# Optimization experiments

Hardware: AMD Instinct MI355X
Metric: run time of the kernel (lower is better)

## Reference

```python
import jax, jax.numpy as jnp
import numpy as np

N_NODES = 100000
N_EDGES = 1250000
D_IN = 64
D_HID = 64
N_CLS = 40


def setup_inputs() -> dict:
    key = jax.random.key(0)
    ks = jax.random.split(key, 8)
    x = jax.random.normal(ks[0], (N_NODES, D_IN), dtype=jnp.float32)
    edge_index = jax.random.randint(ks[1], (2, N_EDGES), 0, N_NODES, dtype=jnp.int64)
    s = 1.0 / np.sqrt(D_IN)
    W1_l = jax.random.normal(ks[2], (D_IN, D_HID), dtype=jnp.float32) * s
    W1_r = jax.random.normal(ks[3], (D_IN, D_HID), dtype=jnp.float32) * s
    b1 = jnp.zeros((D_HID,), dtype=jnp.float32)
    s2 = 1.0 / np.sqrt(D_HID)
    W2_l = jax.random.normal(ks[4], (D_HID, N_CLS), dtype=jnp.float32) * s2
    W2_r = jax.random.normal(ks[5], (D_HID, N_CLS), dtype=jnp.float32) * s2
    b2 = jnp.zeros((N_CLS,), dtype=jnp.float32)
    return {"x": x, "edge_index": edge_index, "W1_l": W1_l, "b1": b1,
            "W1_r": W1_r, "W2_l": W2_l, "b2": b2, "W2_r": W2_r}


def _sage_conv(h, src, dst, n_nodes, W_l, b, W_r):
    # mean-aggregate neighbor features: out[i] = mean_{(j->i)} h[j]
    msg = h[src]                                             # [E, d] gather
    agg = jax.ops.segment_sum(msg, dst, num_segments=n_nodes)  # [N, d] scatter-add
    deg = jax.ops.segment_sum(jnp.ones_like(dst, dtype=h.dtype), dst,
                              num_segments=n_nodes)
    agg = agg / jnp.maximum(deg, 1.0)[:, None]
    # lin_l(aggregated, bias) + lin_r(root, no bias)
    return agg @ W_l + b + h @ W_r


def reference(x, edge_index, W1_l, b1, W1_r, W2_l, b2, W2_r):
    n = x.shape[0]
    src, dst = edge_index[0], edge_index[1]
    h = jax.nn.relu(_sage_conv(x, src, dst, n, W1_l, b1, W1_r))
    # dropout is identity in eval mode (training=False)
    h = _sage_conv(h, src, dst, n, W2_l, b2, W2_r)
    return jax.nn.log_softmax(h, axis=1)
```

## Files before the change

kernel.cpp:

```cpp
#include <hip/hip_runtime.h>
#include <hip/hip_bf16.h>
#include <math.h>

#define N_NODES 100000
#define N_EDGES 1250000
#define D_IN    64
#define D_HID   64
#define N_CLS   40

#define NBUCK      500
#define BUCK_NODES 200
#define BUCK_CAP   2944
#define NBLK_STAGE 512
#define NBLK_GEMM1 1024
#define ELL_W      44

typedef unsigned int uint;
typedef __attribute__((ext_vector_type(8))) short bf16x8;
typedef __attribute__((ext_vector_type(4))) float f32x4;

static __device__ __forceinline__ uint pack_bf16x2(float a, float b) {
    unsigned short ua = __builtin_bit_cast(unsigned short, __float2bfloat16(a));
    unsigned short ub = __builtin_bit_cast(unsigned short, __float2bfloat16(b));
    return (uint)ua | ((uint)ub << 16);
}
static __device__ __forceinline__ short f2bf(float f) {
    return (short)__builtin_bit_cast(unsigned short, __float2bfloat16(f));
}

__global__ __launch_bounds__(256, 3) void stage_and_gemm1(
    const int* __restrict__ src, const int* __restrict__ dst,
    int* __restrict__ bucketCnt, uint* __restrict__ staged,
    const float* __restrict__ x,
    const float* __restrict__ W_l, const float* __restrict__ W_r,
    const float* __restrict__ b,
    __hip_bfloat16* __restrict__ y1, __hip_bfloat16* __restrict__ r1,
    int ntiles)
{
    __shared__ int cntB[NBUCK], offB[NBUCK], gbase[NBUCK];

    if (blockIdx.x < NBLK_STAGE) {
        const int per = (N_EDGES + NBLK_STAGE - 1) / NBLK_STAGE;
        const int e0 = blockIdx.x * per;
        const int e1 = (e0 + per < N_EDGES) ? e0 + per : N_EDGES;
        for (int i = threadIdx.x; i < NBUCK; i += 256) { cntB[i] = 0; offB[i] = 0; }
        __syncthreads();
        for (int e = e0 + threadIdx.x; e < e1; e += 256)
            atomicAdd(&cntB[dst[e] / BUCK_NODES], 1);
        __syncthreads();
        for (int i = threadIdx.x; i < NBUCK; i += 256) {
            int c = cntB[i];
            gbase[i] = c ? atomicAdd(&bucketCnt[i], c) : 0;
        }
        __syncthreads();
        for (int e = e0 + threadIdx.x; e < e1; e += 256) {
            int d = dst[e];
            int s = src[e];
            int bk = d / BUCK_NODES;
            int pos = gbase[bk] + atomicAdd(&offB[bk], 1);
            if (pos < BUCK_CAP)
                staged[(size_t)bk * BUCK_CAP + pos] =
                    (uint)s | ((uint)(d - bk * BUCK_NODES) << 17);
        }
        return;
    }

    const int gbid = blockIdx.x - NBLK_STAGE;
    if (gbid == 0 && threadIdx.x < 64)
        y1[(size_t)N_NODES * 64 + threadIdx.x] = __float2bfloat16(0.0f);

    const int lane = threadIdx.x & 63;
    const int m = lane & 15;
    const int q = lane >> 4;

    bf16x8 bfrag[8][2];
    float  biasv[4];
    #pragma unroll
    for (int t = 0; t < 8; ++t) {
        const float* Wsrc = (t < 4) ? W_l : W_r;
        const int c = t * 16 + m - ((t < 4) ? 0 : 64);
        #pragma unroll
        for (int ks = 0; ks < 2; ++ks) {
            bf16x8 f;
            #pragma unroll
            for (int j = 0; j < 8; ++j)
                f[j] = f2bf(Wsrc[(ks * 32 + q * 8 + j) * 64 + c]);
            bfrag[t][ks] = f;
        }
    }
    #pragma unroll
    for (int t = 0; t < 4; ++t) biasv[t] = b[t * 16 + m];

    int wid = gbid * 4 + (threadIdx.x >> 6);
    const int nw = NBLK_GEMM1 * 4;
    for (int tile = wid; tile < ntiles; tile += nw) {
        const int node0 = tile * 16;
        const float* xrow = x + (size_t)(node0 + m) * 64 + q * 8;
        bf16x8 afrag[2];
        #pragma unroll
        for (int ks = 0; ks < 2; ++ks) {
            float4 f0 = *(const float4*)(xrow + ks * 32);
            float4 f1 = *(const float4*)(xrow + ks * 32 + 4);
            bf16x8 a;
            a[0] = f2bf(f0.x); a[1] = f2bf(f0.y); a[2] = f2bf(f0.z); a[3] = f2bf(f0.w);
            a[4] = f2bf(f1.x); a[5] = f2bf(f1.y); a[6] = f2bf(f1.z); a[7] = f2bf(f1.w);
            afrag[ks] = a;
        }
        f32x4 acc[8];
        #pragma unroll
        for (int t = 0; t < 8; ++t) acc[t] = (f32x4){0.f, 0.f, 0.f, 0.f};
        #pragma unroll
        for (int ks = 0; ks < 2; ++ks) {
            #pragma unroll
            for (int t = 0; t < 8; ++t)
                acc[t] = __builtin_amdgcn_mfma_f32_16x16x32_bf16(
                    afrag[ks], bfrag[t][ks], acc[t], 0, 0, 0);
        }
        #pragma unroll
        for (int t = 0; t < 8; ++t) {
            #pragma unroll
            for (int r = 0; r < 4; ++r) {
                const size_t row = (size_t)(node0 + q * 4 + r);
                if (t < 4)
                    y1[row * 64 + t * 16 + m] = __float2bfloat16(acc[t][r]);
                else
                    r1[row * 64 + (t - 4) * 16 + m] =
                        __float2bfloat16(acc[t][r] + biasv[t - 4]);
            }
        }
    }
}

__global__ __launch_bounds__(256) void ell_fill(
    const uint* __restrict__ staged, const int* __restrict__ bucketCnt,
    int* __restrict__ cnt, int* __restrict__ slots)
{
    __shared__ int lcnt[BUCK_NODES];
    const int b = blockIdx.x;
    const int node0 = b * BUCK_NODES;
    for (int i = threadIdx.x; i < BUCK_NODES; i += 256) lcnt[i] = 0;
    __syncthreads();
    int total = bucketCnt[b];
    if (total > BUCK_CAP) total = BUCK_CAP;
    const uint* sp = staged + (size_t)b * BUCK_CAP;
    for (int i = threadIdx.x; i < total; i += 256) {
        uint v = sp[i];
        int off = (int)(v >> 17);
        int pos = atomicAdd(&lcnt[off], 1);
        if (pos < ELL_W)
            slots[(size_t)(node0 + off) * ELL_W + pos] = (int)(v & 0x1FFFFu);
    }
    __syncthreads();
    for (int i = threadIdx.x; i < BUCK_NODES; i += 256) {
        int node = node0 + i;
        if (node < N_NODES) cnt[node] = lcnt[i];
    }
}

__global__ __launch_bounds__(256, 3) void gemm2_mfma(
    const __hip_bfloat16* __restrict__ h,
    const float* __restrict__ W_l, const float* __restrict__ W_r,
    const float* __restrict__ b,
    __hip_bfloat16* __restrict__ y2, __hip_bfloat16* __restrict__ r2,
    int ntiles)
{
    if (blockIdx.x == 0 && threadIdx.x < N_CLS)
        y2[(size_t)N_NODES * N_CLS + threadIdx.x] = __float2bfloat16(0.0f);

    const int lane = threadIdx.x & 63;
    const int m = lane & 15;
    const int q = lane >> 4;

    bf16x8 bfrag[5][2];
    float  biasv[5];
    #pragma unroll
    for (int t = 0; t < 5; ++t) {
        const int g = t * 16 + m;
        const float* Wsrc = (g < N_CLS) ? W_l : W_r;
        const int c = (g < N_CLS) ? g : g - N_CLS;
        #pragma unroll
        for (int ks = 0; ks < 2; ++ks) {
            bf16x8 f;
            #pragma unroll
            for (int j = 0; j < 8; ++j)
                f[j] = f2bf(Wsrc[(ks * 32 + q * 8 + j) * N_CLS + c]);
            bfrag[t][ks] = f;
        }
        biasv[t] = (g >= N_CLS) ? b[g - N_CLS] : 0.0f;
    }

    int wid = blockIdx.x * 4 + (threadIdx.x >> 6);
    const int nw = gridDim.x * 4;
    for (int tile = wid; tile < ntiles; tile += nw) {
        const int node0 = tile * 16;
        const __hip_bfloat16* hrow = h + (size_t)(node0 + m) * 64 + q * 8;
        bf16x8 afrag[2];
        afrag[0] = *(const bf16x8*)(hrow);
        afrag[1] = *(const bf16x8*)(hrow + 32);
        f32x4 acc[5];
        #pragma unroll
        for (int t = 0; t < 5; ++t) acc[t] = (f32x4){0.f, 0.f, 0.f, 0.f};
        #pragma unroll
        for (int ks = 0; ks < 2; ++ks) {
            #pragma unroll
            for (int t = 0; t < 5; ++t)
                acc[t] = __builtin_amdgcn_mfma_f32_16x16x32_bf16(
                    afrag[ks], bfrag[t][ks], acc[t], 0, 0, 0);
        }
        #pragma unroll
        for (int t = 0; t < 5; ++t) {
            const int g = t * 16 + m;
            #pragma unroll
            for (int r = 0; r < 4; ++r) {
                const size_t row = (size_t)(node0 + q * 4 + r);
                float v = acc[t][r] + biasv[t];
                if (g < N_CLS) y2[row * N_CLS + g] = __float2bfloat16(v);
                else           r2[row * N_CLS + (g - N_CLS)] = __float2bfloat16(v);
            }
        }
    }
}

__global__ __launch_bounds__(256, 8) void gather1(
    const __hip_bfloat16* __restrict__ y1,
    const int* __restrict__ cnt, const int* __restrict__ slots,
    __hip_bfloat16* __restrict__ h,
    int n_nodes)
{
    const int lane = threadIdx.x & 63;
    const int q4  = (lane >> 4) * 4;
    const int pre = (lane & 15) * 8;
    const char* y1c = (const char*)y1;

    const int wave = blockIdx.x * 4 + (threadIdx.x >> 6);
    const int nw   = gridDim.x * 4;

    int node = wave;
    if (node >= n_nodes) return;
    int degr = cnt[node];
    int idxv = slots[node * ELL_W + lane];

    for (;;) {
        const int nnode = node + nw;
        int ndeg = 0, nidx = 0;
        if (nnode < n_nodes) {
            ndeg = cnt[nnode];
            nidx = slots[nnode * ELL_W + lane];
        }

        const int degc = degr < ELL_W ? degr : ELL_W;
        int idx = (lane >= degc) ? n_nodes : idxv;
        float a0 = 0.f, a1 = 0.f, a2 = 0.f, a3 = 0.f;
        const int groups = (degc + 15) & ~15;
        for (int e = 0; e < groups; e += 16) {
            int sel0 = __builtin_amdgcn_ds_bpermute(e * 4      + q4, idx);
            int sel1 = __builtin_amdgcn_ds_bpermute(e * 4 + 16 + q4, idx);
            int sel2 = __builtin_amdgcn_ds_bpermute(e * 4 + 32 + q4, idx);
            int sel3 = __builtin_amdgcn_ds_bpermute(e * 4 + 48 + q4, idx);
            uint2 d0 = *(const uint2*)(y1c + ((size_t)(uint)sel0 * 128u + (uint)pre));
            uint2 d1 = *(const uint2*)(y1c + ((size_t)(uint)sel1 * 128u + (uint)pre));
            uint2 d2 = *(const uint2*)(y1c + ((size_t)(uint)sel2 * 128u + (uint)pre));
            uint2 d3 = *(const uint2*)(y1c + ((size_t)(uint)sel3 * 128u + (uint)pre));
            a0 += __uint_as_float(d0.x << 16) + __uint_as_float(d1.x << 16)
                + __uint_as_float(d2.x << 16) + __uint_as_float(d3.x << 16);
            a1 += __uint_as_float(d0.x & 0xffff0000u) + __uint_as_float(d1.x & 0xffff0000u)
                + __uint_as_float(d2.x & 0xffff0000u) + __uint_as_float(d3.x & 0xffff0000u);
            a2 += __uint_as_float(d0.y << 16) + __uint_as_float(d1.y << 16)
                + __uint_as_float(d2.y << 16) + __uint_as_float(d3.y << 16);
            a3 += __uint_as_float(d0.y & 0xffff0000u) + __uint_as_float(d1.y & 0xffff0000u)
                + __uint_as_float(d2.y & 0xffff0000u) + __uint_as_float(d3.y & 0xffff0000u);
        }
        a0 += __shfl_xor(a0, 16); a0 += __shfl_xor(a0, 32);
        a1 += __shfl_xor(a1, 16); a1 += __shfl_xor(a1, 32);
        a2 += __shfl_xor(a2, 16); a2 += __shfl_xor(a2, 32);
        a3 += __shfl_xor(a3, 16); a3 += __shfl_xor(a3, 32);

        uint2 rr = *(const uint2*)((const char*)h + ((size_t)node * 128u + (uint)pre));
        float r0  = __uint_as_float(rr.x << 16);
        float r1v = __uint_as_float(rr.x & 0xffff0000u);
        float r2v = __uint_as_float(rr.y << 16);
        float r3  = __uint_as_float(rr.y & 0xffff0000u);

        float inv = 1.0f / (float)(degr > 1 ? degr : 1);
        float v0 = a0 * inv + r0;  v0 = v0 > 0.f ? v0 : 0.f;
        float v1 = a1 * inv + r1v; v1 = v1 > 0.f ? v1 : 0.f;
        float v2 = a2 * inv + r2v; v2 = v2 > 0.f ? v2 : 0.f;
        float v3 = a3 * inv + r3;  v3 = v3 > 0.f ? v3 : 0.f;

        if (lane < 16) {
            uint2 o;
            o.x = pack_bf16x2(v0, v1);
            o.y = pack_bf16x2(v2, v3);
            *(uint2*)((char*)h + ((size_t)node * 128u + (uint)pre)) = o;
        }

        if (nnode >= n_nodes) break;
        node = nnode; degr = ndeg; idxv = nidx;
    }
}

__global__ __launch_bounds__(256, 8) void gather2(
    const __hip_bfloat16* __restrict__ y2,
    const __hip_bfloat16* __restrict__ r2,
    const int* __restrict__ cnt, const int* __restrict__ slots,
    float* __restrict__ out, int n_nodes)
{
    const int lane  = threadIdx.x & 63;
    const int lpair = lane & 31;
    const int p2    = (lane >> 5) * 4;
    const int pre2  = (lpair < 20 ? lpair : 19) * 4;
    const char* y2c = (const char*)y2;

    const int wave = blockIdx.x * 4 + (threadIdx.x >> 6);
    const int nw   = gridDim.x * 4;

    int node = wave;
    if (node >= n_nodes) return;
    int degr = cnt[node];
    int idxv = slots[node * ELL_W + lane];

    for (;;) {
        const int nnode = node + nw;
        int ndeg = 0, nidx = 0;
        if (nnode < n_nodes) {
            ndeg = cnt[nnode];
            nidx = slots[nnode * ELL_W + lane];
        }

        const int degc = degr < ELL_W ? degr : ELL_W;
        int idx = (lane >= degc) ? n_nodes : idxv;
        float a0 = 0.f, a1 = 0.f;
        const int groups = (degc + 7) & ~7;
        for (int e = 0; e < groups; e += 8) {
            int sel0 = __builtin_amdgcn_ds_bpermute(e * 4      + p2, idx);
            int sel1 = __builtin_amdgcn_ds_bpermute(e * 4 +  8 + p2, idx);
            int sel2 = __builtin_amdgcn_ds_bpermute(e * 4 + 16 + p2, idx);
            int sel3 = __builtin_amdgcn_ds_bpermute(e * 4 + 24 + p2, idx);
            uint d0 = *(const uint*)(y2c + ((size_t)(uint)sel0 * 80u + (uint)pre2));
            uint d1 = *(const uint*)(y2c + ((size_t)(uint)sel1 * 80u + (uint)pre2));
            uint d2 = *(const uint*)(y2c + ((size_t)(uint)sel2 * 80u + (uint)pre2));
            uint d3 = *(const uint*)(y2c + ((size_t)(uint)sel3 * 80u + (uint)pre2));
            a0 += __uint_as_float(d0 << 16) + __uint_as_float(d1 << 16)
                + __uint_as_float(d2 << 16) + __uint_as_float(d3 << 16);
            a1 += __uint_as_float(d0 & 0xffff0000u) + __uint_as_float(d1 & 0xffff0000u)
                + __uint_as_float(d2 & 0xffff0000u) + __uint_as_float(d3 & 0xffff0000u);
        }
        a0 += __shfl_xor(a0, 32);
        a1 += __shfl_xor(a1, 32);

        uint rr = *(const uint*)((const char*)r2 + ((size_t)node * 80u + (uint)pre2));
        float r0 = __uint_as_float(rr << 16);
        float r1 = __uint_as_float(rr & 0xffff0000u);

        float inv = 1.0f / (float)(degr > 1 ? degr : 1);
        float l0 = a0 * inv + r0;
        float l1 = a1 * inv + r1;
        if (lpair >= 20) { l0 = -INFINITY; l1 = -INFINITY; }

        float m = fmaxf(l0, l1);
        #pragma unroll
        for (int off = 16; off > 0; off >>= 1)
            m = fmaxf(m, __shfl_xor(m, off));
        float ex = (lpair < 20) ? (expf(l0 - m) + expf(l1 - m)) : 0.0f;
        #pragma unroll
        for (int off = 16; off > 0; off >>= 1)
            ex += __shfl_xor(ex, off);
        float lg = m + logf(ex);
        if (lane < 20) {
            float2 o = make_float2(l0 - lg, l1 - lg);
            *(float2*)(out + (size_t)node * N_CLS + lpair * 2) = o;
        }

        if (nnode >= n_nodes) break;
        node = nnode; degr = ndeg; idxv = nidx;
    }
}

extern "C" void kernel_launch(void* const* d_in, const int* in_sizes, int n_in,
                              void* d_out, int out_size, void* d_ws, size_t ws_size,
                              hipStream_t stream)
{
    (void)in_sizes; (void)n_in; (void)out_size; (void)ws_size;

    const float* x    = (const float*)d_in[0];
    const int*   ei   = (const int*)d_in[1];
    const float* W1_l = (const float*)d_in[2];
    const float* b1   = (const float*)d_in[3];
    const float* W1_r = (const float*)d_in[4];
    const float* W2_l = (const float*)d_in[5];
    const float* b2   = (const float*)d_in[6];
    const float* W2_r = (const float*)d_in[7];
    float* out = (float*)d_out;

    const int* src = ei;
    const int* dst = ei + N_EDGES;

    char* ws = (char*)d_ws;
    int*            cnt       = (int*)(ws);
    int*            bucketCnt = (int*)(ws + 400000);
    int*            slots     = (int*)(ws + (1u << 20));
    __hip_bfloat16* y1        = (__hip_bfloat16*)(ws + 19922944u);
    __hip_bfloat16* y2        = (__hip_bfloat16*)(ws + 19922944u);
    __hip_bfloat16* h         = (__hip_bfloat16*)(ws + 34603008u);
    uint*           staged    = (uint*)(ws + 48234496u);
    __hip_bfloat16* r2        = (__hip_bfloat16*)(ws + 48234496u);

    const int ntiles = N_NODES / 16;

    hipMemsetAsync(bucketCnt, 0, NBUCK * sizeof(int), stream);
    stage_and_gemm1<<<NBLK_STAGE + NBLK_GEMM1, 256, 0, stream>>>(
        src, dst, bucketCnt, staged, x, W1_l, W1_r, b1, y1, h, ntiles);

    ell_fill<<<NBUCK, 256, 0, stream>>>(staged, bucketCnt, cnt, slots);

    gather1<<<2048, 256, 0, stream>>>(y1, cnt, slots, h, N_NODES);

    gemm2_mfma<<<1024, 256, 0, stream>>>(h, W2_l, W2_r, b2, y2, r2, ntiles);

    gather2<<<2048, 256, 0, stream>>>(y2, r2, cnt, slots, out, N_NODES);
}
```

Measured before the change: 208.8 us.

## Build ELL adjacency directly with global atomics, dropping bucket staging pass

Replaces the two-stage bucketed staging plus ell_fill kernel with a direct build: each thread loads several edges and does a global atomicAdd on the per-node count to claim an ELL slot, then writes the source index. This removes one kernel launch, the staged intermediate buffer round-trip, and the per-block shared-memory bucketing. In exchange it issues 1.25M global atomics with scattered slot writes, and the count array must be zeroed by a larger memset.

```diff
diff --git a/kernel.cpp b/kernel.cpp
--- a/kernel.cpp
+++ b/kernel.cpp
@@ -8,12 +8,10 @@
 #define D_HID   64
 #define N_CLS   40
 
-#define NBUCK      500
-#define BUCK_NODES 200
-#define BUCK_CAP   2944
-#define NBLK_STAGE 512
-#define NBLK_GEMM1 1024
-#define ELL_W      44
+#define NBLK_BUILD  1024
+#define NBLK_GEMM1  1024
+#define EDGE_UNROLL 5
+#define ELL_W       44
 
 typedef unsigned int uint;
 typedef __attribute__((ext_vector_type(8))) short bf16x8;
@@ -28,44 +26,37 @@
     return (short)__builtin_bit_cast(unsigned short, __float2bfloat16(f));
 }
 
-__global__ __launch_bounds__(256, 3) void stage_and_gemm1(
+__global__ __launch_bounds__(256, 3) void build_and_gemm1(
     const int* __restrict__ src, const int* __restrict__ dst,
-    int* __restrict__ bucketCnt, uint* __restrict__ staged,
+    int* __restrict__ cnt, int* __restrict__ slots,
     const float* __restrict__ x,
     const float* __restrict__ W_l, const float* __restrict__ W_r,
     const float* __restrict__ b,
     __hip_bfloat16* __restrict__ y1, __hip_bfloat16* __restrict__ r1,
     int ntiles)
 {
-    __shared__ int cntB[NBUCK], offB[NBUCK], gbase[NBUCK];
-
-    if (blockIdx.x < NBLK_STAGE) {
-        const int per = (N_EDGES + NBLK_STAGE - 1) / NBLK_STAGE;
-        const int e0 = blockIdx.x * per;
-        const int e1 = (e0 + per < N_EDGES) ? e0 + per : N_EDGES;
-        for (int i = threadIdx.x; i < NBUCK; i += 256) { cntB[i] = 0; offB[i] = 0; }
-        __syncthreads();
-        for (int e = e0 + threadIdx.x; e < e1; e += 256)
-            atomicAdd(&cntB[dst[e] / BUCK_NODES], 1);
-        __syncthreads();
-        for (int i = threadIdx.x; i < NBUCK; i += 256) {
-            int c = cntB[i];
-            gbase[i] = c ? atomicAdd(&bucketCnt[i], c) : 0;
-        }
-        __syncthreads();
-        for (int e = e0 + threadIdx.x; e < e1; e += 256) {
-            int d = dst[e];
-            int s = src[e];
-            int bk = d / BUCK_NODES;
-            int pos = gbase[bk] + atomicAdd(&offB[bk], 1);
-            if (pos < BUCK_CAP)
-                staged[(size_t)bk * BUCK_CAP + pos] =
-                    (uint)s | ((uint)(d - bk * BUCK_NODES) << 17);
-        }
+    if (blockIdx.x < NBLK_BUILD) {
+        const int tid = blockIdx.x * 256 + threadIdx.x;
+        const int nth = NBLK_BUILD * 256;
+        int d[EDGE_UNROLL], s[EDGE_UNROLL], p[EDGE_UNROLL];
+        #pragma unroll
+        for (int i = 0; i < EDGE_UNROLL; ++i) {
+            const int e = tid + i * nth;
+            const bool ok = (e < N_EDGES);
+            d[i] = ok ? dst[e] : -1;
+            s[i] = ok ? src[e] : 0;
+        }
+        #pragma unroll
+        for (int i = 0; i < EDGE_UNROLL; ++i)
+            p[i] = (d[i] >= 0) ? atomicAdd(&cnt[d[i]], 1) : ELL_W;
+        #pragma unroll
+        for (int i = 0; i < EDGE_UNROLL; ++i)
+            if (p[i] < ELL_W)
+                slots[(size_t)d[i] * ELL_W + p[i]] = s[i];
         return;
     }
 
-    const int gbid = blockIdx.x - NBLK_STAGE;
+    const int gbid = blockIdx.x - NBLK_BUILD;
     if (gbid == 0 && threadIdx.x < 64)
         y1[(size_t)N_NODES * 64 + threadIdx.x] = __float2bfloat16(0.0f);
 
@@ -128,32 +119,6 @@
                         __float2bfloat16(acc[t][r] + biasv[t - 4]);
             }
         }
-    }
-}
-
-__global__ __launch_bounds__(256) void ell_fill(
-    const uint* __restrict__ staged, const int* __restrict__ bucketCnt,
-    int* __restrict__ cnt, int* __restrict__ slots)
-{
-    __shared__ int lcnt[BUCK_NODES];
-    const int b = blockIdx.x;
-    const int node0 = b * BUCK_NODES;
-    for (int i = threadIdx.x; i < BUCK_NODES; i += 256) lcnt[i] = 0;
-    __syncthreads();
-    int total = bucketCnt[b];
-    if (total > BUCK_CAP) total = BUCK_CAP;
-    const uint* sp = staged + (size_t)b * BUCK_CAP;
-    for (int i = threadIdx.x; i < total; i += 256) {
-        uint v = sp[i];
-        int off = (int)(v >> 17);
-        int pos = atomicAdd(&lcnt[off], 1);
-        if (pos < ELL_W)
-            slots[(size_t)(node0 + off) * ELL_W + pos] = (int)(v & 0x1FFFFu);
-    }
-    __syncthreads();
-    for (int i = threadIdx.x; i < BUCK_NODES; i += 256) {
-        int node = node0 + i;
-        if (node < N_NODES) cnt[node] = lcnt[i];
     }
 }
 
@@ -397,21 +362,17 @@
 
     char* ws = (char*)d_ws;
     int*            cnt       = (int*)(ws);
-    int*            bucketCnt = (int*)(ws + 400000);
     int*            slots     = (int*)(ws + (1u << 20));
     __hip_bfloat16* y1        = (__hip_bfloat16*)(ws + 19922944u);
     __hip_bfloat16* y2        = (__hip_bfloat16*)(ws + 19922944u);
     __hip_bfloat16* h         = (__hip_bfloat16*)(ws + 34603008u);
-    uint*           staged    = (uint*)(ws + 48234496u);
     __hip_bfloat16* r2        = (__hip_bfloat16*)(ws + 48234496u);
 
     const int ntiles = N_NODES / 16;
 
-    hipMemsetAsync(bucketCnt, 0, NBUCK * sizeof(int), stream);
-    stage_and_gemm1<<<NBLK_STAGE + NBLK_GEMM1, 256, 0, stream>>>(
-        src, dst, bucketCnt, staged, x, W1_l, W1_r, b1, y1, h, ntiles);
-
-    ell_fill<<<NBUCK, 256, 0, stream>>>(staged, bucketCnt, cnt, slots);
+    hipMemsetAsync(cnt, 0, N_NODES * sizeof(int), stream);
+    build_and_gemm1<<<NBLK_BUILD + NBLK_GEMM1, 256, 0, stream>>>(
+        src, dst, cnt, slots, x, W1_l, W1_r, b1, y1, h, ntiles);
 
     gather1<<<2048, 256, 0, stream>>>(y1, cnt, slots, h, N_NODES);
 
```

After: 238.7 us. 14.3% more time.

## Fuse ELL construction into gather kernels using per-block shared-memory adjacency

Applied to the files above, without the earlier changes.

Removes the separate ell_fill kernel and the global cnt/slots arrays. Each gather kernel block now rebuilds the adjacency for its 100 nodes in shared memory from the staged bucket data, then runs the neighbor gather out of LDS. This saves a launch and the global write and read of the ELL arrays. In exchange, each bucket's staged edges are scanned twice per layer (two half-blocks), the build is repeated in both layers, and the fixed 1000-block grid loses the persistent prefetching loop.

```diff
diff --git a/kernel.cpp b/kernel.cpp
--- a/kernel.cpp
+++ b/kernel.cpp
@@ -14,6 +14,7 @@
 #define NBLK_STAGE 512
 #define NBLK_GEMM1 1024
 #define ELL_W      44
+#define GNODES     100
 
 typedef unsigned int uint;
 typedef __attribute__((ext_vector_type(8))) short bf16x8;
@@ -131,125 +132,46 @@
     }
 }
 
-__global__ __launch_bounds__(256) void ell_fill(
+__global__ __launch_bounds__(512) void bucket_gather1(
+    const __hip_bfloat16* __restrict__ y1,
     const uint* __restrict__ staged, const int* __restrict__ bucketCnt,
-    int* __restrict__ cnt, int* __restrict__ slots)
+    __hip_bfloat16* __restrict__ h)
 {
-    __shared__ int lcnt[BUCK_NODES];
-    const int b = blockIdx.x;
-    const int node0 = b * BUCK_NODES;
-    for (int i = threadIdx.x; i < BUCK_NODES; i += 256) lcnt[i] = 0;
+    __shared__ int lcnt[GNODES];
+    __shared__ int lslots[GNODES * ELL_W + 64];
+    const int pb = blockIdx.x >> 1;
+    const int hf = blockIdx.x & 1;
+    const int node0 = pb * BUCK_NODES + hf * GNODES;
+
+    for (int i = threadIdx.x; i < GNODES; i += 512) lcnt[i] = 0;
     __syncthreads();
-    int total = bucketCnt[b];
-    if (total > BUCK_CAP) total = BUCK_CAP;
-    const uint* sp = staged + (size_t)b * BUCK_CAP;
-    for (int i = threadIdx.x; i < total; i += 256) {
+
+    int total = bucketCnt[pb]; if (total > BUCK_CAP) total = BUCK_CAP;
+    const uint* sp = staged + (size_t)pb * BUCK_CAP;
+    const int rel0 = hf * GNODES;
+    for (int i = threadIdx.x; i < total; i += 512) {
         uint v = sp[i];
-        int off = (int)(v >> 17);
-        int pos = atomicAdd(&lcnt[off], 1);
-        if (pos < ELL_W)
-            slots[(size_t)(node0 + off) * ELL_W + pos] = (int)(v & 0x1FFFFu);
+        int rel = (int)(v >> 17) - rel0;
+        if (0 <= rel && rel < GNODES) {
+            int pos = atomicAdd(&lcnt[rel], 1);
+            if (pos < ELL_W) lslots[rel * ELL_W + pos] = (int)(v & 0x1FFFFu);
+        }
     }
     __syncthreads();
-    for (int i = threadIdx.x; i < BUCK_NODES; i += 256) {
-        int node = node0 + i;
-        if (node < N_NODES) cnt[node] = lcnt[i];
-    }
-}
-
-__global__ __launch_bounds__(256, 3) void gemm2_mfma(
-    const __hip_bfloat16* __restrict__ h,
-    const float* __restrict__ W_l, const float* __restrict__ W_r,
-    const float* __restrict__ b,
-    __hip_bfloat16* __restrict__ y2, __hip_bfloat16* __restrict__ r2,
-    int ntiles)
-{
-    if (blockIdx.x == 0 && threadIdx.x < N_CLS)
-        y2[(size_t)N_NODES * N_CLS + threadIdx.x] = __float2bfloat16(0.0f);
 
     const int lane = threadIdx.x & 63;
-    const int m = lane & 15;
-    const int q = lane >> 4;
-
-    bf16x8 bfrag[5][2];
-    float  biasv[5];
-    #pragma unroll
-    for (int t = 0; t < 5; ++t) {
-        const int g = t * 16 + m;
-        const float* Wsrc = (g < N_CLS) ? W_l : W_r;
-        const int c = (g < N_CLS) ? g : g - N_CLS;
-        #pragma unroll
-        for (int ks = 0; ks < 2; ++ks) {
-            bf16x8 f;
-            #pragma unroll
-            for (int j = 0; j < 8; ++j)
-                f[j] = f2bf(Wsrc[(ks * 32 + q * 8 + j) * N_CLS + c]);
-            bfrag[t][ks] = f;
-        }
-        biasv[t] = (g >= N_CLS) ? b[g - N_CLS] : 0.0f;
-    }
-
-    int wid = blockIdx.x * 4 + (threadIdx.x >> 6);
-    const int nw = gridDim.x * 4;
-    for (int tile = wid; tile < ntiles; tile += nw) {
-        const int node0 = tile * 16;
-        const __hip_bfloat16* hrow = h + (size_t)(node0 + m) * 64 + q * 8;
-        bf16x8 afrag[2];
-        afrag[0] = *(const bf16x8*)(hrow);
-        afrag[1] = *(const bf16x8*)(hrow + 32);
-        f32x4 acc[5];
-        #pragma unroll
-        for (int t = 0; t < 5; ++t) acc[t] = (f32x4){0.f, 0.f, 0.f, 0.f};
-        #pragma unroll
-        for (int ks = 0; ks < 2; ++ks) {
-            #pragma unroll
-            for (int t = 0; t < 5; ++t)
-                acc[t] = __builtin_amdgcn_mfma_f32_16x16x32_bf16(
-                    afrag[ks], bfrag[t][ks], acc[t], 0, 0, 0);
-        }
-        #pragma unroll
-        for (int t = 0; t < 5; ++t) {
-            const int g = t * 16 + m;
-            #pragma unroll
-            for (int r = 0; r < 4; ++r) {
-                const size_t row = (size_t)(node0 + q * 4 + r);
-                float v = acc[t][r] + biasv[t];
-                if (g < N_CLS) y2[row * N_CLS + g] = __float2bfloat16(v);
-                else           r2[row * N_CLS + (g - N_CLS)] = __float2bfloat16(v);
-            }
-        }
-    }
-}
-
-__global__ __launch_bounds__(256, 8) void gather1(
-    const __hip_bfloat16* __restrict__ y1,
-    const int* __restrict__ cnt, const int* __restrict__ slots,
-    __hip_bfloat16* __restrict__ h,
-    int n_nodes)
-{
-    const int lane = threadIdx.x & 63;
-    const int q4  = (lane >> 4) * 4;
-    const int pre = (lane & 15) * 8;
+    const int wv   = threadIdx.x >> 6;
+    const int q4   = (lane >> 4) * 4;
+    const int pre  = (lane & 15) * 8;
     const char* y1c = (const char*)y1;
 
-    const int wave = blockIdx.x * 4 + (threadIdx.x >> 6);
-    const int nw   = gridDim.x * 4;
-
-    int node = wave;
-    if (node >= n_nodes) return;
-    int degr = cnt[node];
-    int idxv = slots[node * ELL_W + lane];
-
-    for (;;) {
-        const int nnode = node + nw;
-        int ndeg = 0, nidx = 0;
-        if (nnode < n_nodes) {
-            ndeg = cnt[nnode];
-            nidx = slots[nnode * ELL_W + lane];
-        }
-
+    for (int n = wv; n < GNODES; n += 8) {
+        const int node = node0 + n;
+        const int degr = lcnt[n];
+        const int idxv = lslots[n * ELL_W + lane];
         const int degc = degr < ELL_W ? degr : ELL_W;
-        int idx = (lane >= degc) ? n_nodes : idxv;
+        int idx = (lane >= degc) ? N_NODES : idxv;
+
         float a0 = 0.f, a1 = 0.f, a2 = 0.f, a3 = 0.f;
         const int groups = (degc + 15) & ~15;
         for (int e = 0; e < groups; e += 16) {
@@ -293,42 +215,115 @@
             o.y = pack_bf16x2(v2, v3);
             *(uint2*)((char*)h + ((size_t)node * 128u + (uint)pre)) = o;
         }
-
-        if (nnode >= n_nodes) break;
-        node = nnode; degr = ndeg; idxv = nidx;
-    }
-}
-
-__global__ __launch_bounds__(256, 8) void gather2(
+    }
+}
+
+__global__ __launch_bounds__(256, 3) void gemm2_mfma(
+    const __hip_bfloat16* __restrict__ h,
+    const float* __restrict__ W_l, const float* __restrict__ W_r,
+    const float* __restrict__ b,
+    __hip_bfloat16* __restrict__ y2, __hip_bfloat16* __restrict__ r2,
+    int ntiles)
+{
+    if (blockIdx.x == 0 && threadIdx.x < N_CLS)
+        y2[(size_t)N_NODES * N_CLS + threadIdx.x] = __float2bfloat16(0.0f);
+
+    const int lane = threadIdx.x & 63;
+    const int m = lane & 15;
+    const int q = lane >> 4;
+
+    bf16x8 bfrag[5][2];
+    float  biasv[5];
+    #pragma unroll
+    for (int t = 0; t < 5; ++t) {
+        const int g = t * 16 + m;
+        const float* Wsrc = (g < N_CLS) ? W_l : W_r;
+        const int c = (g < N_CLS) ? g : g - N_CLS;
+        #pragma unroll
+        for (int ks = 0; ks < 2; ++ks) {
+            bf16x8 f;
+            #pragma unroll
+            for (int j = 0; j < 8; ++j)
+                f[j] = f2bf(Wsrc[(ks * 32 + q * 8 + j) * N_CLS + c]);
+            bfrag[t][ks] = f;
+        }
+        biasv[t] = (g >= N_CLS) ? b[g - N_CLS] : 0.0f;
+    }
+
+    int wid = blockIdx.x * 4 + (threadIdx.x >> 6);
+    const int nw = gridDim.x * 4;
+    for (int tile = wid; tile < ntiles; tile += nw) {
+        const int node0 = tile * 16;
+        const __hip_bfloat16* hrow = h + (size_t)(node0 + m) * 64 + q * 8;
+        bf16x8 afrag[2];
+        afrag[0] = *(const bf16x8*)(hrow);
+        afrag[1] = *(const bf16x8*)(hrow + 32);
+        f32x4 acc[5];
+        #pragma unroll
+        for (int t = 0; t < 5; ++t) acc[t] = (f32x4){0.f, 0.f, 0.f, 0.f};
+        #pragma unroll
+        for (int ks = 0; ks < 2; ++ks) {
+            #pragma unroll
+            for (int t = 0; t < 5; ++t)
+                acc[t] = __builtin_amdgcn_mfma_f32_16x16x32_bf16(
+                    afrag[ks], bfrag[t][ks], acc[t], 0, 0, 0);
+        }
+        #pragma unroll
+        for (int t = 0; t < 5; ++t) {
+            const int g = t * 16 + m;
+            #pragma unroll
+            for (int r = 0; r < 4; ++r) {
+                const size_t row = (size_t)(node0 + q * 4 + r);
+                float v = acc[t][r] + biasv[t];
+                if (g < N_CLS) y2[row * N_CLS + g] = __float2bfloat16(v);
+                else           r2[row * N_CLS + (g - N_CLS)] = __float2bfloat16(v);
+            }
+        }
+    }
+}
+
+__global__ __launch_bounds__(512) void bucket_gather2(
     const __hip_bfloat16* __restrict__ y2,
     const __hip_bfloat16* __restrict__ r2,
-    const int* __restrict__ cnt, const int* __restrict__ slots,
-    float* __restrict__ out, int n_nodes)
+    const uint* __restrict__ staged, const int* __restrict__ bucketCnt,
+    float* __restrict__ out)
 {
+    __shared__ int lcnt[GNODES];
+    __shared__ int lslots[GNODES * ELL_W + 64];
+    const int pb = blockIdx.x >> 1;
+    const int hf = blockIdx.x & 1;
+    const int node0 = pb * BUCK_NODES + hf * GNODES;
+
+    for (int i = threadIdx.x; i < GNODES; i += 512) lcnt[i] = 0;
+    __syncthreads();
+
+    int total = bucketCnt[pb]; if (total > BUCK_CAP) total = BUCK_CAP;
+    const uint* sp = staged + (size_t)pb * BUCK_CAP;
+    const int rel0 = hf * GNODES;
+    for (int i = threadIdx.x; i < total; i += 512) {
+        uint v = sp[i];
+        int rel = (int)(v >> 17) - rel0;
+        if (0 <= rel && rel < GNODES) {
+            int pos = atomicAdd(&lcnt[rel], 1);
+            if (pos < ELL_W) lslots[rel * ELL_W + pos] = (int)(v & 0x1FFFFu);
+        }
+    }
+    __syncthreads();
+
     const int lane  = threadIdx.x & 63;
+    const int wv    = threadIdx.x >> 6;
     const int lpair = lane & 31;
     const int p2    = (lane >> 5) * 4;
-    const int pre2  = (lpair < 20 ? lpair : 19) * 4;
+    const uint pre2 = (uint)(lpair < 20 ? lpair : 19) * 4u;
     const char* y2c = (const char*)y2;
 
-    const int wave = blockIdx.x * 4 + (threadIdx.x >> 6);
-    const int nw   = gridDim.x * 4;
-
-    int node = wave;
-    if (node >= n_nodes) return;
-    int degr = cnt[node];
-    int idxv = slots[node * ELL_W + lane];
-
-    for (;;) {
-        const int nnode = node + nw;
-        int ndeg = 0, nidx = 0;
-        if (nnode < n_nodes) {
-            ndeg = cnt[nnode];
-            nidx = slots[nnode * ELL_W + lane];
-        }
-
+    for (int n = wv; n < GNODES; n += 8) {
+        const int node = node0 + n;
+        const int degr = lcnt[n];
+        const int idxv = lslots[n * ELL_W + lane];
         const int degc = degr < ELL_W ? degr : ELL_W;
-        int idx = (lane >= degc) ? n_nodes : idxv;
+        int idx = (lane >= degc) ? N_NODES : idxv;
+
         float a0 = 0.f, a1 = 0.f;
         const int groups = (degc + 7) & ~7;
         for (int e = 0; e < groups; e += 8) {
@@ -336,10 +331,10 @@
             int sel1 = __builtin_amdgcn_ds_bpermute(e * 4 +  8 + p2, idx);
             int sel2 = __builtin_amdgcn_ds_bpermute(e * 4 + 16 + p2, idx);
             int sel3 = __builtin_amdgcn_ds_bpermute(e * 4 + 24 + p2, idx);
-            uint d0 = *(const uint*)(y2c + ((size_t)(uint)sel0 * 80u + (uint)pre2));
-            uint d1 = *(const uint*)(y2c + ((size_t)(uint)sel1 * 80u + (uint)pre2));
-            uint d2 = *(const uint*)(y2c + ((size_t)(uint)sel2 * 80u + (uint)pre2));
-            uint d3 = *(const uint*)(y2c + ((size_t)(uint)sel3 * 80u + (uint)pre2));
+            uint d0 = *(const uint*)(y2c + ((size_t)(uint)sel0 * 80u + pre2));
+            uint d1 = *(const uint*)(y2c + ((size_t)(uint)sel1 * 80u + pre2));
+            uint d2 = *(const uint*)(y2c + ((size_t)(uint)sel2 * 80u + pre2));
+            uint d3 = *(const uint*)(y2c + ((size_t)(uint)sel3 * 80u + pre2));
             a0 += __uint_as_float(d0 << 16) + __uint_as_float(d1 << 16)
                 + __uint_as_float(d2 << 16) + __uint_as_float(d3 << 16);
             a1 += __uint_as_float(d0 & 0xffff0000u) + __uint_as_float(d1 & 0xffff0000u)
@@ -348,7 +343,7 @@
         a0 += __shfl_xor(a0, 32);
         a1 += __shfl_xor(a1, 32);
 
-        uint rr = *(const uint*)((const char*)r2 + ((size_t)node * 80u + (uint)pre2));
+        uint rr = *(const uint*)((const char*)r2 + ((size_t)node * 80u + pre2));
         float r0 = __uint_as_float(rr << 16);
         float r1 = __uint_as_float(rr & 0xffff0000u);
 
@@ -370,9 +365,6 @@
             float2 o = make_float2(l0 - lg, l1 - lg);
             *(float2*)(out + (size_t)node * N_CLS + lpair * 2) = o;
         }
-
-        if (nnode >= n_nodes) break;
-        node = nnode; degr = ndeg; idxv = nidx;
     }
 }
 
@@ -396,14 +388,12 @@
     const int* dst = ei + N_EDGES;
 
     char* ws = (char*)d_ws;
-    int*            cnt       = (int*)(ws);
-    int*            bucketCnt = (int*)(ws + 400000);
-    int*            slots     = (int*)(ws + (1u << 20));
-    __hip_bfloat16* y1        = (__hip_bfloat16*)(ws + 19922944u);
-    __hip_bfloat16* y2        = (__hip_bfloat16*)(ws + 19922944u);
-    __hip_bfloat16* h         = (__hip_bfloat16*)(ws + 34603008u);
-    uint*           staged    = (uint*)(ws + 48234496u);
-    __hip_bfloat16* r2        = (__hip_bfloat16*)(ws + 48234496u);
+    int*            bucketCnt = (int*)(ws);
+    uint*           staged    = (uint*)(ws + (1u << 20));
+    __hip_bfloat16* y1        = (__hip_bfloat16*)(ws + 8388608u);
+    __hip_bfloat16* y2        = (__hip_bfloat16*)(ws + 8388608u);
+    __hip_bfloat16* h         = (__hip_bfloat16*)(ws + 22020096u);
+    __hip_bfloat16* r2        = (__hip_bfloat16*)(ws + 35651584u);
 
     const int ntiles = N_NODES / 16;
 
@@ -411,11 +401,9 @@
     stage_and_gemm1<<<NBLK_STAGE + NBLK_GEMM1, 256, 0, stream>>>(
         src, dst, bucketCnt, staged, x, W1_l, W1_r, b1, y1, h, ntiles);
 
-    ell_fill<<<NBUCK, 256, 0, stream>>>(staged, bucketCnt, cnt, slots);
-
-    gather1<<<2048, 256, 0, stream>>>(y1, cnt, slots, h, N_NODES);
+    bucket_gather1<<<NBUCK * 2, 512, 0, stream>>>(y1, staged, bucketCnt, h);
 
     gemm2_mfma<<<1024, 256, 0, stream>>>(h, W2_l, W2_r, b2, y2, r2, ntiles);
 
-    gather2<<<2048, 256, 0, stream>>>(y2, r2, cnt, slots, out, N_NODES);
-}
+    bucket_gather2<<<NBUCK * 2, 512, 0, stream>>>(y2, r2, staged, bucketCnt, out);
+}
```

New measurement: 194.0 us. 1.08x faster.
